# Kernel tuning notes

Hardware: AMD Instinct MI355X
Metric: run time of the kernel (lower is better)

## Reference

```python
import jax, jax.numpy as jnp
import numpy as np

# Hyperparameters (match init_kwargs)
COORD_DIM = 3
GRID_MIN = -1.0
GRID_MAX = 1.0
N_LEVELS = 16
N_FEATS = 2
LOG2_T = 19
TABLE_SIZE = 2 ** LOG2_T
BASE_RES = 16
FINEST_RES = 512
BSZ = 1048576

_growth = np.exp((np.log(FINEST_RES) - np.log(BASE_RES)) / (N_LEVELS - 1))
RESOLUTIONS = [int(np.floor(BASE_RES * _growth ** i)) for i in range(N_LEVELS)]

# InstantNGP spatial-hash primes (uint32: low bits of the product/xor are
# identical to the int64 computation, and we only keep LOG2_T low bits).
PRIMES = jnp.asarray(np.array([1, 2654435761, 805459861], dtype=np.uint32))
# (8, 3) binary corner offsets of a unit cube.
OFFSETS = jnp.asarray(
    np.array([[(k >> d) & 1 for d in range(COORD_DIM)] for k in range(2 ** COORD_DIM)],
             dtype=np.uint32))
MASK = jnp.uint32(TABLE_SIZE - 1)


def _embed_level(x, table, resolution):
    """x: (B, 3) coords; table: (T, F) hash table. Returns (B, F)."""
    grid_size = (GRID_MAX - GRID_MIN) / resolution
    rel = (x - GRID_MIN) / grid_size                       # (B, 3)
    idx0 = jnp.clip(jnp.floor(rel), 0, resolution - 1)     # bottom-left vertex index
    w = rel - idx0                                         # (B, 3) interp weights in [0,1]
    vidx = idx0.astype(jnp.uint32)[:, None, :] + OFFSETS[None]   # (B, 8, 3)
    # spatial hash: xor of (index * prime) over dims, masked to table size
    vp = vidx * PRIMES[None, None, :]
    h = (vp[..., 0] ^ vp[..., 1] ^ vp[..., 2]) & MASK      # (B, 8) uint32
    verts = table[h.astype(jnp.int32)]                      # (B, 8, F) gather
    # d-linear interpolation weights per corner
    wts = jnp.prod(jnp.where(OFFSETS[None] == 1, w[:, None, :], 1.0 - w[:, None, :]),
                   axis=-1)                                 # (B, 8)
    return jnp.einsum('bv,bvf->bf', wts, verts)             # (B, F)


def setup_inputs() -> dict:
    k1, k2 = jax.random.split(jax.random.key(0))
    x = jax.random.uniform(k1, (BSZ, COORD_DIM), jnp.float32,
                           minval=GRID_MIN, maxval=GRID_MAX)
    embeddings = jax.random.uniform(k2, (N_LEVELS, TABLE_SIZE, N_FEATS), jnp.float32,
                                    minval=-1e-4, maxval=1e-4)
    return {"x": x, "embeddings": embeddings}


def reference(x, embeddings):
    outs = [_embed_level(x, embeddings[i], RESOLUTIONS[i]) for i in range(N_LEVELS)]
    return jnp.concatenate(outs, axis=-1)  # (B, L*F)
```

## Files before the change

kernel.cpp:

```cpp
#include <hip/hip_runtime.h>
#include <hip/hip_fp16.h>
#include <stdint.h>


#define N_LEVELS   16
#define LOG2_T     19
#define TABLE_SIZE (1u << LOG2_T)
#define HASH_MASK  (TABLE_SIZE - 1u)
#define P1 2654435761u
#define P2 805459861u
#define N_DENSE    8

__constant__ int   c_res[N_LEVELS]   = {16, 20, 25, 32, 40, 50, 64, 80,
                                        101, 128, 161, 203, 256, 322, 406, 512};
__constant__ float c_scale[N_LEVELS] = {8.0f, 10.0f, 12.5f, 16.0f, 20.0f, 25.0f,
                                        32.0f, 40.0f, 50.5f, 64.0f, 80.5f, 101.5f,
                                        128.0f, 161.0f, 203.0f, 256.0f};

__constant__ uint32_t c_dim[N_DENSE]  = {17, 21, 26, 33, 41, 51, 65, 81};
__constant__ uint32_t c_doff[N_DENSE] = {0, 4913, 14174, 31750,
                                         67687, 136608, 269259, 543884};
#define DENSE_TOTAL 1075325u

__constant__ uint32_t c_coff[N_DENSE] = {0, 4096, 12096, 27721,
                                         60489, 124489, 249489, 511633};
#define CELL_TOTAL 1023633u

__global__ __launch_bounds__(256) void conv_hash(
    const float2* __restrict__ emb, uint32_t* __restrict__ ht, int total)
{
    int i = blockIdx.x * 256 + threadIdx.x;
    if (i >= total) return;
    float2 v = emb[(size_t)N_DENSE * TABLE_SIZE + i];
    __half2 h = __float22half2_rn(v);
    ht[i] = *(uint32_t*)&h;
}

__global__ __launch_bounds__(256) void conv_cell(
    const float2* __restrict__ emb, uint4* __restrict__ cg)
{
    int l = blockIdx.y;
    uint32_t c = blockIdx.x * 256 + threadIdx.x;
    uint32_t R = (uint32_t)c_res[l];
    if (c >= R * R * R) return;
    uint32_t ix = c % R;
    uint32_t r  = c / R;
    uint32_t iy = r % R;
    uint32_t iz = r / R;

    const float2* __restrict__ tb = emb + (size_t)l * TABLE_SIZE;
    uint32_t a0 = ix,      a1 = ix + 1u;
    uint32_t b0 = iy * P1, b1 = b0 + P1;
    uint32_t d0 = iz * P2, d1 = d0 + P2;

    float2 f0 = tb[(a0 ^ b0 ^ d0) & HASH_MASK];
    float2 f1 = tb[(a1 ^ b0 ^ d0) & HASH_MASK];
    float2 f2 = tb[(a0 ^ b1 ^ d0) & HASH_MASK];
    float2 f3 = tb[(a1 ^ b1 ^ d0) & HASH_MASK];
    float2 f4 = tb[(a0 ^ b0 ^ d1) & HASH_MASK];
    float2 f5 = tb[(a1 ^ b0 ^ d1) & HASH_MASK];
    float2 f6 = tb[(a0 ^ b1 ^ d1) & HASH_MASK];
    float2 f7 = tb[(a1 ^ b1 ^ d1) & HASH_MASK];

    __half2 h0 = __float22half2_rn(f0), h1 = __float22half2_rn(f1);
    __half2 h2 = __float22half2_rn(f2), h3 = __float22half2_rn(f3);
    __half2 h4 = __float22half2_rn(f4), h5 = __float22half2_rn(f5);
    __half2 h6 = __float22half2_rn(f6), h7 = __float22half2_rn(f7);

    uint32_t base = 2u * (c_coff[l] + c);
    cg[base]      = make_uint4(*(uint32_t*)&h0, *(uint32_t*)&h1,
                               *(uint32_t*)&h2, *(uint32_t*)&h3);
    cg[base + 1u] = make_uint4(*(uint32_t*)&h4, *(uint32_t*)&h5,
                               *(uint32_t*)&h6, *(uint32_t*)&h7);
}

__global__ __launch_bounds__(256) void conv_dense(
    const float2* __restrict__ emb, uint32_t* __restrict__ dn)
{
    int l = blockIdx.y;
    uint32_t v = blockIdx.x * 256 + threadIdx.x;
    uint32_t S = c_dim[l];
    if (v >= S * S * S) return;
    uint32_t ix = v % S;
    uint32_t r  = v / S;
    uint32_t iy = r % S;
    uint32_t iz = r / S;
    uint32_t h  = (ix ^ (iy * P1) ^ (iz * P2)) & HASH_MASK;
    float2 val  = emb[(size_t)l * TABLE_SIZE + h];
    __half2 hv  = __float22half2_rn(val);
    dn[c_doff[l] + v] = *(uint32_t*)&hv;
}

template <bool CELL>
__device__ __forceinline__ void do_point(
    int l, int b, int npts,
    const float* __restrict__ x,
    const uint32_t* __restrict__ ht,
    const uint32_t* __restrict__ dn,
    const uint4*    __restrict__ cg,
    uint32_t* __restrict__ tmp)
{
    if (b >= npts) return;
    size_t xb = (size_t)b * 3;
    float xx = x[xb], xy = x[xb + 1], xz = x[xb + 2];

    float scale = c_scale[l];
    float hiv   = (float)c_res[l] - 1.0f;

    float rx = (xx + 1.0f) * scale;
    float ry = (xy + 1.0f) * scale;
    float rz = (xz + 1.0f) * scale;

    float fx = fminf(fmaxf(floorf(rx), 0.0f), hiv);
    float fy = fminf(fmaxf(floorf(ry), 0.0f), hiv);
    float fz = fminf(fmaxf(floorf(rz), 0.0f), hiv);

    float wx = rx - fx, wy = ry - fy, wz = rz - fz;
    uint32_t ix = (uint32_t)fx, iy = (uint32_t)fy, iz = (uint32_t)fz;

    uint32_t u0, u1, u2, u3, u4, u5, u6, u7;
    if (l < N_DENSE) {
        if constexpr (CELL) {
            uint32_t R    = (uint32_t)c_res[l];
            uint32_t cidx = (iz * R + iy) * R + ix;
            uint32_t base = 2u * (c_coff[l] + cidx);
            uint4 lo = cg[base];
            uint4 hi = cg[base + 1u];
            u0 = lo.x; u1 = lo.y; u2 = lo.z; u3 = lo.w;
            u4 = hi.x; u5 = hi.y; u6 = hi.z; u7 = hi.w;
        } else {
            uint32_t S    = c_dim[l];
            uint32_t base = c_doff[l] + (iz * S + iy) * S + ix;
            uint32_t S2   = S * S;
            u0 = dn[base];           u1 = dn[base + 1];
            u2 = dn[base + S];       u3 = dn[base + S + 1];
            u4 = dn[base + S2];      u5 = dn[base + S2 + 1];
            u6 = dn[base + S2 + S];  u7 = dn[base + S2 + S + 1];
        }
    } else {
        const uint32_t* __restrict__ tb = ht + (size_t)(l - N_DENSE) * TABLE_SIZE;
        uint32_t a0 = ix,      a1 = ix + 1u;
        uint32_t b0 = iy * P1, b1 = b0 + P1;
        uint32_t c0 = iz * P2, c1 = c0 + P2;
        u0 = tb[(a0 ^ b0 ^ c0) & HASH_MASK];
        u1 = tb[(a1 ^ b0 ^ c0) & HASH_MASK];
        u2 = tb[(a0 ^ b1 ^ c0) & HASH_MASK];
        u3 = tb[(a1 ^ b1 ^ c0) & HASH_MASK];
        u4 = tb[(a0 ^ b0 ^ c1) & HASH_MASK];
        u5 = tb[(a1 ^ b0 ^ c1) & HASH_MASK];
        u6 = tb[(a0 ^ b1 ^ c1) & HASH_MASK];
        u7 = tb[(a1 ^ b1 ^ c1) & HASH_MASK];
    }

    float2 v0 = __half22float2(*(__half2*)&u0);
    float2 v1 = __half22float2(*(__half2*)&u1);
    float2 v2 = __half22float2(*(__half2*)&u2);
    float2 v3 = __half22float2(*(__half2*)&u3);
    float2 v4 = __half22float2(*(__half2*)&u4);
    float2 v5 = __half22float2(*(__half2*)&u5);
    float2 v6 = __half22float2(*(__half2*)&u6);
    float2 v7 = __half22float2(*(__half2*)&u7);

    float ux = 1.0f - wx, uy = 1.0f - wy, uz = 1.0f - wz;
    float w0 = ux * uy * uz, w1 = wx * uy * uz;
    float w2 = ux * wy * uz, w3 = wx * wy * uz;
    float w4 = ux * uy * wz, w5 = wx * uy * wz;
    float w6 = ux * wy * wz, w7 = wx * wy * wz;

    float o0 = w0 * v0.x + w1 * v1.x + w2 * v2.x + w3 * v3.x
             + w4 * v4.x + w5 * v5.x + w6 * v6.x + w7 * v7.x;
    float o1 = w0 * v0.y + w1 * v1.y + w2 * v2.y + w3 * v3.y
             + w4 * v4.y + w5 * v5.y + w6 * v6.y + w7 * v7.y;

    __half2 r = __float22half2_rn(make_float2(o0, o1));
    tmp[(size_t)l * npts + b] = *(uint32_t*)&r;
}

template <bool CELL>
__global__ __launch_bounds__(256) void gather_lvl(
    const float* __restrict__ x,
    const uint32_t* __restrict__ ht,
    const uint32_t* __restrict__ dn,
    const uint4*    __restrict__ cg,
    uint32_t* __restrict__ tmp, int npts)
{
    const int l  = blockIdx.y;
    const int bA = blockIdx.x * 512 + threadIdx.x;
    do_point<CELL>(l, bA,       npts, x, ht, dn, cg, tmp);
    do_point<CELL>(l, bA + 256, npts, x, ht, dn, cg, tmp);
}

__global__ __launch_bounds__(256) void transpose_k(
    const uint32_t* __restrict__ tmp, float4* __restrict__ out4, int npts)
{
    __shared__ uint32_t sm[N_LEVELS][514];

    const int b0 = blockIdx.x * 512;
    const int t  = threadIdx.x;

    if (b0 + 512 <= npts) {
        #pragma unroll
        for (int l = 0; l < N_LEVELS; ++l) {
            uint2 u = *(const uint2*)&tmp[(size_t)l * npts + b0 + 2 * t];
            *(uint2*)&sm[l][2 * t] = u;
        }
        __syncthreads();
        #pragma unroll
        for (int k = 0; k < 16; ++k) {
            int q = k * 256 + t;
            int p = q >> 3;
            int j = q & 7;
            uint32_t a = sm[2 * j][p], b = sm[2 * j + 1][p];
            float2 f0 = __half22float2(*(__half2*)&a);
            float2 f1 = __half22float2(*(__half2*)&b);
            out4[(size_t)(b0 + p) * 8 + j] = make_float4(f0.x, f0.y, f1.x, f1.y);
        }
    } else {
        for (int l = 0; l < N_LEVELS; ++l) {
            for (int s = 0; s < 2; ++s) {
                int b = b0 + 2 * t + s;
                if (b < npts) sm[l][2 * t + s] = tmp[(size_t)l * npts + b];
            }
        }
        __syncthreads();
        for (int k = 0; k < 16; ++k) {
            int q = k * 256 + t;
            int p = q >> 3, j = q & 7;
            if (b0 + p < npts) {
                uint32_t a = sm[2 * j][p], b = sm[2 * j + 1][p];
                float2 f0 = __half22float2(*(__half2*)&a);
                float2 f1 = __half22float2(*(__half2*)&b);
                out4[(size_t)(b0 + p) * 8 + j] = make_float4(f0.x, f0.y, f1.x, f1.y);
            }
        }
    }
}

__global__ __launch_bounds__(256) void hash_embed_direct(
    const float* __restrict__ x, const float* __restrict__ emb,
    float2* __restrict__ out, int npts)
{
    int t = blockIdx.x * 256 + threadIdx.x;
    int l = t & 15, b = t >> 4;
    if (b >= npts) return;
    size_t xb = (size_t)b * 3;
    float scale = c_scale[l], hiv = (float)c_res[l] - 1.0f;
    float rx = (x[xb] + 1.0f) * scale, ry = (x[xb+1] + 1.0f) * scale, rz = (x[xb+2] + 1.0f) * scale;
    float fx = fminf(fmaxf(floorf(rx), 0.0f), hiv);
    float fy = fminf(fmaxf(floorf(ry), 0.0f), hiv);
    float fz = fminf(fmaxf(floorf(rz), 0.0f), hiv);
    float wx = rx - fx, wy = ry - fy, wz = rz - fz;
    uint32_t ix = (uint32_t)fx, iy = (uint32_t)fy, iz = (uint32_t)fz;
    uint32_t a0 = ix, a1 = ix + 1u, b0 = iy * P1, b1 = b0 + P1, c0 = iz * P2, c1 = c0 + P2;
    const float2* tb = (const float2*)emb + (size_t)l * TABLE_SIZE;
    float2 v0 = tb[(a0^b0^c0)&HASH_MASK], v1 = tb[(a1^b0^c0)&HASH_MASK];
    float2 v2 = tb[(a0^b1^c0)&HASH_MASK], v3 = tb[(a1^b1^c0)&HASH_MASK];
    float2 v4 = tb[(a0^b0^c1)&HASH_MASK], v5 = tb[(a1^b0^c1)&HASH_MASK];
    float2 v6 = tb[(a0^b1^c1)&HASH_MASK], v7 = tb[(a1^b1^c1)&HASH_MASK];
    float ux = 1.0f - wx, uy = 1.0f - wy, uz = 1.0f - wz;
    float w0 = ux*uy*uz, w1 = wx*uy*uz, w2 = ux*wy*uz, w3 = wx*wy*uz;
    float w4 = ux*uy*wz, w5 = wx*uy*wz, w6 = ux*wy*wz, w7 = wx*wy*wz;
    float o0 = w0*v0.x+w1*v1.x+w2*v2.x+w3*v3.x+w4*v4.x+w5*v5.x+w6*v6.x+w7*v7.x;
    float o1 = w0*v0.y+w1*v1.y+w2*v2.y+w3*v3.y+w4*v4.y+w5*v5.y+w6*v6.y+w7*v7.y;
    out[(size_t)b * N_LEVELS + l] = make_float2(o0, o1);
}

extern "C" void kernel_launch(void* const* d_in, const int* in_sizes, int n_in,
                              void* d_out, int out_size, void* d_ws, size_t ws_size,
                              hipStream_t stream)
{
    const float*  x   = (const float*)d_in[0];
    const float2* emb = (const float2*)d_in[1];
    int npts = in_sizes[0] / 3;

    size_t tmp_bytes = (size_t)npts * N_LEVELS * 4;
    size_t ht_bytes  = (size_t)N_DENSE * TABLE_SIZE * 4;
    size_t cg_bytes  = (size_t)CELL_TOTAL * 32;
    size_t dn_bytes  = (size_t)DENSE_TOTAL * 4;

    int ht_total = N_DENSE * TABLE_SIZE;

    if (ws_size >= tmp_bytes + ht_bytes + cg_bytes) {
        uint32_t* tmp = (uint32_t*)d_ws;
        uint32_t* ht  = (uint32_t*)((char*)d_ws + tmp_bytes);
        uint4*    cg  = (uint4*)   ((char*)d_ws + tmp_bytes + ht_bytes);

        hipLaunchKernelGGL(conv_hash, dim3((ht_total + 255) / 256), dim3(256),
                           0, stream, emb, ht, ht_total);
        hipLaunchKernelGGL(conv_cell, dim3(2000, N_DENSE), dim3(256),
                           0, stream, emb, cg);
        hipLaunchKernelGGL(HIP_KERNEL_NAME(gather_lvl<true>),
                           dim3((npts + 511) / 512, N_LEVELS), dim3(256),
                           0, stream, x, ht, (const uint32_t*)nullptr, cg, tmp, npts);
        hipLaunchKernelGGL(transpose_k, dim3((npts + 511) / 512), dim3(256),
                           0, stream, tmp, (float4*)d_out, npts);
    } else if (ws_size >= tmp_bytes + ht_bytes + dn_bytes) {
        uint32_t* tmp = (uint32_t*)d_ws;
        uint32_t* ht  = (uint32_t*)((char*)d_ws + tmp_bytes);
        uint32_t* dn  = (uint32_t*)((char*)d_ws + tmp_bytes + ht_bytes);

        hipLaunchKernelGGL(conv_hash, dim3((ht_total + 255) / 256), dim3(256),
                           0, stream, emb, ht, ht_total);
        hipLaunchKernelGGL(conv_dense, dim3(2077, N_DENSE), dim3(256),
                           0, stream, emb, dn);
        hipLaunchKernelGGL(HIP_KERNEL_NAME(gather_lvl<false>),
                           dim3((npts + 511) / 512, N_LEVELS), dim3(256),
                           0, stream, x, ht, dn, (const uint4*)nullptr, tmp, npts);
        hipLaunchKernelGGL(transpose_k, dim3((npts + 511) / 512), dim3(256),
                           0, stream, tmp, (float4*)d_out, npts);
    } else {
        int total = npts * N_LEVELS;
        hipLaunchKernelGGL(hash_embed_direct, dim3((total + 255) / 256), dim3(256),
                           0, stream, (const float*)x, (const float*)emb,
                           (float2*)d_out, npts);
    }
}
```

Before: 460.1 us.

## Fuse per-level gather and transpose into one per-point kernel over all levels

```diff
diff --git a/kernel.cpp b/kernel.cpp
--- a/kernel.cpp
+++ b/kernel.cpp
@@ -11,20 +11,20 @@
 #define P2 805459861u
 #define N_DENSE    8
 
-__constant__ int   c_res[N_LEVELS]   = {16, 20, 25, 32, 40, 50, 64, 80,
-                                        101, 128, 161, 203, 256, 322, 406, 512};
-__constant__ float c_scale[N_LEVELS] = {8.0f, 10.0f, 12.5f, 16.0f, 20.0f, 25.0f,
-                                        32.0f, 40.0f, 50.5f, 64.0f, 80.5f, 101.5f,
-                                        128.0f, 161.0f, 203.0f, 256.0f};
-
-__constant__ uint32_t c_dim[N_DENSE]  = {17, 21, 26, 33, 41, 51, 65, 81};
-__constant__ uint32_t c_doff[N_DENSE] = {0, 4913, 14174, 31750,
-                                         67687, 136608, 269259, 543884};
-#define DENSE_TOTAL 1075325u
-
+typedef float  fx4 __attribute__((ext_vector_type(4)));
+
+__constant__ int   c_res[N_DENSE]   = {16, 20, 25, 32, 40, 50, 64, 80};
 __constant__ uint32_t c_coff[N_DENSE] = {0, 4096, 12096, 27721,
                                          60489, 124489, 249489, 511633};
 #define CELL_TOTAL 1023633u
+
+constexpr int      kRes[N_LEVELS]   = {16, 20, 25, 32, 40, 50, 64, 80,
+                                       101, 128, 161, 203, 256, 322, 406, 512};
+constexpr float    kScale[N_LEVELS] = {8.0f, 10.0f, 12.5f, 16.0f, 20.0f, 25.0f,
+                                       32.0f, 40.0f, 50.5f, 64.0f, 80.5f, 101.5f,
+                                       128.0f, 161.0f, 203.0f, 256.0f};
+constexpr uint32_t kCoff[N_DENSE]   = {0, 4096, 12096, 27721,
+                                       60489, 124489, 249489, 511633};
 
 __global__ __launch_bounds__(256) void conv_hash(
     const float2* __restrict__ emb, uint32_t* __restrict__ ht, int total)
@@ -74,164 +74,90 @@
                                *(uint32_t*)&h6, *(uint32_t*)&h7);
 }
 
-__global__ __launch_bounds__(256) void conv_dense(
-    const float2* __restrict__ emb, uint32_t* __restrict__ dn)
-{
-    int l = blockIdx.y;
-    uint32_t v = blockIdx.x * 256 + threadIdx.x;
-    uint32_t S = c_dim[l];
-    if (v >= S * S * S) return;
-    uint32_t ix = v % S;
-    uint32_t r  = v / S;
-    uint32_t iy = r % S;
-    uint32_t iz = r / S;
-    uint32_t h  = (ix ^ (iy * P1) ^ (iz * P2)) & HASH_MASK;
-    float2 val  = emb[(size_t)l * TABLE_SIZE + h];
-    __half2 hv  = __float22half2_rn(val);
-    dn[c_doff[l] + v] = *(uint32_t*)&hv;
-}
-
-template <bool CELL>
-__device__ __forceinline__ void do_point(
-    int l, int b, int npts,
+__global__ __launch_bounds__(256) void gather_all(
     const float* __restrict__ x,
     const uint32_t* __restrict__ ht,
-    const uint32_t* __restrict__ dn,
     const uint4*    __restrict__ cg,
-    uint32_t* __restrict__ tmp)
-{
+    float*          __restrict__ out, int npts)
+{
+    int b = blockIdx.x * 256 + threadIdx.x;
     if (b >= npts) return;
+
     size_t xb = (size_t)b * 3;
     float xx = x[xb], xy = x[xb + 1], xz = x[xb + 2];
 
-    float scale = c_scale[l];
-    float hiv   = (float)c_res[l] - 1.0f;
-
-    float rx = (xx + 1.0f) * scale;
-    float ry = (xy + 1.0f) * scale;
-    float rz = (xz + 1.0f) * scale;
-
-    float fx = fminf(fmaxf(floorf(rx), 0.0f), hiv);
-    float fy = fminf(fmaxf(floorf(ry), 0.0f), hiv);
-    float fz = fminf(fmaxf(floorf(rz), 0.0f), hiv);
-
-    float wx = rx - fx, wy = ry - fy, wz = rz - fz;
-    uint32_t ix = (uint32_t)fx, iy = (uint32_t)fy, iz = (uint32_t)fz;
-
-    uint32_t u0, u1, u2, u3, u4, u5, u6, u7;
-    if (l < N_DENSE) {
-        if constexpr (CELL) {
-            uint32_t R    = (uint32_t)c_res[l];
-            uint32_t cidx = (iz * R + iy) * R + ix;
-            uint32_t base = 2u * (c_coff[l] + cidx);
+    float e0 = 0.0f, e1 = 0.0f;
+
+    #pragma unroll
+    for (int l = 0; l < N_LEVELS; ++l) {
+        const float scale = kScale[l];
+        const float hiv   = (float)kRes[l] - 1.0f;
+
+        float rx = (xx + 1.0f) * scale;
+        float ry = (xy + 1.0f) * scale;
+        float rz = (xz + 1.0f) * scale;
+
+        float fx = fminf(fmaxf(floorf(rx), 0.0f), hiv);
+        float fy = fminf(fmaxf(floorf(ry), 0.0f), hiv);
+        float fz = fminf(fmaxf(floorf(rz), 0.0f), hiv);
+
+        float wx = rx - fx, wy = ry - fy, wz = rz - fz;
+        uint32_t ix = (uint32_t)fx, iy = (uint32_t)fy, iz = (uint32_t)fz;
+
+        uint32_t u0, u1, u2, u3, u4, u5, u6, u7;
+        if (l < N_DENSE) {
+            const uint32_t R    = (uint32_t)kRes[l];
+            const uint32_t cidx = (iz * R + iy) * R + ix;
+            const uint32_t base = 2u * (kCoff[l] + cidx);
             uint4 lo = cg[base];
             uint4 hi = cg[base + 1u];
             u0 = lo.x; u1 = lo.y; u2 = lo.z; u3 = lo.w;
             u4 = hi.x; u5 = hi.y; u6 = hi.z; u7 = hi.w;
         } else {
-            uint32_t S    = c_dim[l];
-            uint32_t base = c_doff[l] + (iz * S + iy) * S + ix;
-            uint32_t S2   = S * S;
-            u0 = dn[base];           u1 = dn[base + 1];
-            u2 = dn[base + S];       u3 = dn[base + S + 1];
-            u4 = dn[base + S2];      u5 = dn[base + S2 + 1];
-            u6 = dn[base + S2 + S];  u7 = dn[base + S2 + S + 1];
+            const uint32_t* __restrict__ tb =
+                ht + (size_t)(l - N_DENSE) * TABLE_SIZE;
+            uint32_t a0 = ix,      a1 = ix + 1u;
+            uint32_t b0 = iy * P1, b1 = b0 + P1;
+            uint32_t c0 = iz * P2, c1 = c0 + P2;
+            u0 = tb[(a0 ^ b0 ^ c0) & HASH_MASK];
+            u1 = tb[(a1 ^ b0 ^ c0) & HASH_MASK];
+            u2 = tb[(a0 ^ b1 ^ c0) & HASH_MASK];
+            u3 = tb[(a1 ^ b1 ^ c0) & HASH_MASK];
+            u4 = tb[(a0 ^ b0 ^ c1) & HASH_MASK];
+            u5 = tb[(a1 ^ b0 ^ c1) & HASH_MASK];
+            u6 = tb[(a0 ^ b1 ^ c1) & HASH_MASK];
+            u7 = tb[(a1 ^ b1 ^ c1) & HASH_MASK];
         }
-    } else {
-        const uint32_t* __restrict__ tb = ht + (size_t)(l - N_DENSE) * TABLE_SIZE;
-        uint32_t a0 = ix,      a1 = ix + 1u;
-        uint32_t b0 = iy * P1, b1 = b0 + P1;
-        uint32_t c0 = iz * P2, c1 = c0 + P2;
-        u0 = tb[(a0 ^ b0 ^ c0) & HASH_MASK];
-        u1 = tb[(a1 ^ b0 ^ c0) & HASH_MASK];
-        u2 = tb[(a0 ^ b1 ^ c0) & HASH_MASK];
-        u3 = tb[(a1 ^ b1 ^ c0) & HASH_MASK];
-        u4 = tb[(a0 ^ b0 ^ c1) & HASH_MASK];
-        u5 = tb[(a1 ^ b0 ^ c1) & HASH_MASK];
-        u6 = tb[(a0 ^ b1 ^ c1) & HASH_MASK];
-        u7 = tb[(a1 ^ b1 ^ c1) & HASH_MASK];
-    }
-
-    float2 v0 = __half22float2(*(__half2*)&u0);
-    float2 v1 = __half22float2(*(__half2*)&u1);
-    float2 v2 = __half22float2(*(__half2*)&u2);
-    float2 v3 = __half22float2(*(__half2*)&u3);
-    float2 v4 = __half22float2(*(__half2*)&u4);
-    float2 v5 = __half22float2(*(__half2*)&u5);
-    float2 v6 = __half22float2(*(__half2*)&u6);
-    float2 v7 = __half22float2(*(__half2*)&u7);
-
-    float ux = 1.0f - wx, uy = 1.0f - wy, uz = 1.0f - wz;
-    float w0 = ux * uy * uz, w1 = wx * uy * uz;
-    float w2 = ux * wy * uz, w3 = wx * wy * uz;
-    float w4 = ux * uy * wz, w5 = wx * uy * wz;
-    float w6 = ux * wy * wz, w7 = wx * wy * wz;
-
-    float o0 = w0 * v0.x + w1 * v1.x + w2 * v2.x + w3 * v3.x
-             + w4 * v4.x + w5 * v5.x + w6 * v6.x + w7 * v7.x;
-    float o1 = w0 * v0.y + w1 * v1.y + w2 * v2.y + w3 * v3.y
-             + w4 * v4.y + w5 * v5.y + w6 * v6.y + w7 * v7.y;
-
-    __half2 r = __float22half2_rn(make_float2(o0, o1));
-    tmp[(size_t)l * npts + b] = *(uint32_t*)&r;
-}
-
-template <bool CELL>
-__global__ __launch_bounds__(256) void gather_lvl(
-    const float* __restrict__ x,
-    const uint32_t* __restrict__ ht,
-    const uint32_t* __restrict__ dn,
-    const uint4*    __restrict__ cg,
-    uint32_t* __restrict__ tmp, int npts)
-{
-    const int l  = blockIdx.y;
-    const int bA = blockIdx.x * 512 + threadIdx.x;
-    do_point<CELL>(l, bA,       npts, x, ht, dn, cg, tmp);
-    do_point<CELL>(l, bA + 256, npts, x, ht, dn, cg, tmp);
-}
-
-__global__ __launch_bounds__(256) void transpose_k(
-    const uint32_t* __restrict__ tmp, float4* __restrict__ out4, int npts)
-{
-    __shared__ uint32_t sm[N_LEVELS][514];
-
-    const int b0 = blockIdx.x * 512;
-    const int t  = threadIdx.x;
-
-    if (b0 + 512 <= npts) {
-        #pragma unroll
-        for (int l = 0; l < N_LEVELS; ++l) {
-            uint2 u = *(const uint2*)&tmp[(size_t)l * npts + b0 + 2 * t];
-            *(uint2*)&sm[l][2 * t] = u;
-        }
-        __syncthreads();
-        #pragma unroll
-        for (int k = 0; k < 16; ++k) {
-            int q = k * 256 + t;
-            int p = q >> 3;
-            int j = q & 7;
-            uint32_t a = sm[2 * j][p], b = sm[2 * j + 1][p];
-            float2 f0 = __half22float2(*(__half2*)&a);
-            float2 f1 = __half22float2(*(__half2*)&b);
-            out4[(size_t)(b0 + p) * 8 + j] = make_float4(f0.x, f0.y, f1.x, f1.y);
-        }
-    } else {
-        for (int l = 0; l < N_LEVELS; ++l) {
-            for (int s = 0; s < 2; ++s) {
-                int b = b0 + 2 * t + s;
-                if (b < npts) sm[l][2 * t + s] = tmp[(size_t)l * npts + b];
-            }
-        }
-        __syncthreads();
-        for (int k = 0; k < 16; ++k) {
-            int q = k * 256 + t;
-            int p = q >> 3, j = q & 7;
-            if (b0 + p < npts) {
-                uint32_t a = sm[2 * j][p], b = sm[2 * j + 1][p];
-                float2 f0 = __half22float2(*(__half2*)&a);
-                float2 f1 = __half22float2(*(__half2*)&b);
-                out4[(size_t)(b0 + p) * 8 + j] = make_float4(f0.x, f0.y, f1.x, f1.y);
-            }
+
+        float2 v0 = __half22float2(*(__half2*)&u0);
+        float2 v1 = __half22float2(*(__half2*)&u1);
+        float2 v2 = __half22float2(*(__half2*)&u2);
+        float2 v3 = __half22float2(*(__half2*)&u3);
+        float2 v4 = __half22float2(*(__half2*)&u4);
+        float2 v5 = __half22float2(*(__half2*)&u5);
+        float2 v6 = __half22float2(*(__half2*)&u6);
+        float2 v7 = __half22float2(*(__half2*)&u7);
+
+        float ux = 1.0f - wx, uy = 1.0f - wy, uz = 1.0f - wz;
+        float w0 = ux * uy * uz, w1 = wx * uy * uz;
+        float w2 = ux * wy * uz, w3 = wx * wy * uz;
+        float w4 = ux * uy * wz, w5 = wx * uy * wz;
+        float w6 = ux * wy * wz, w7 = wx * wy * wz;
+
+        float o0 = w0 * v0.x + w1 * v1.x + w2 * v2.x + w3 * v3.x
+                 + w4 * v4.x + w5 * v5.x + w6 * v6.x + w7 * v7.x;
+        float o1 = w0 * v0.y + w1 * v1.y + w2 * v2.y + w3 * v3.y
+                 + w4 * v4.y + w5 * v5.y + w6 * v6.y + w7 * v7.y;
+
+        __half2 hr = __float22half2_rn(make_float2(o0, o1));
+        float2 fr = __half22float2(hr);
+
+        if (l & 1) {
+            fx4 v; v.x = e0; v.y = e1; v.z = fr.x; v.w = fr.y;
+            __builtin_nontemporal_store(
+                v, (fx4*)(out + (size_t)b * 32 + (l >> 1) * 4));
+        } else {
+            e0 = fr.x; e1 = fr.y;
         }
     }
 }
@@ -244,7 +170,12 @@
     int l = t & 15, b = t >> 4;
     if (b >= npts) return;
     size_t xb = (size_t)b * 3;
-    float scale = c_scale[l], hiv = (float)c_res[l] - 1.0f;
+    constexpr float kS[16] = {8.0f, 10.0f, 12.5f, 16.0f, 20.0f, 25.0f,
+                              32.0f, 40.0f, 50.5f, 64.0f, 80.5f, 101.5f,
+                              128.0f, 161.0f, 203.0f, 256.0f};
+    constexpr int   kR[16] = {16, 20, 25, 32, 40, 50, 64, 80,
+                              101, 128, 161, 203, 256, 322, 406, 512};
+    float scale = kS[l], hiv = (float)kR[l] - 1.0f;
     float rx = (x[xb] + 1.0f) * scale, ry = (x[xb+1] + 1.0f) * scale, rz = (x[xb+2] + 1.0f) * scale;
     float fx = fminf(fmaxf(floorf(rx), 0.0f), hiv);
     float fy = fminf(fmaxf(floorf(ry), 0.0f), hiv);
@@ -273,41 +204,20 @@
     const float2* emb = (const float2*)d_in[1];
     int npts = in_sizes[0] / 3;
 
-    size_t tmp_bytes = (size_t)npts * N_LEVELS * 4;
-    size_t ht_bytes  = (size_t)N_DENSE * TABLE_SIZE * 4;
-    size_t cg_bytes  = (size_t)CELL_TOTAL * 32;
-    size_t dn_bytes  = (size_t)DENSE_TOTAL * 4;
-
+    size_t ht_bytes = (size_t)N_DENSE * TABLE_SIZE * 4;
+    size_t cg_bytes = (size_t)CELL_TOTAL * 32;
     int ht_total = N_DENSE * TABLE_SIZE;
 
-    if (ws_size >= tmp_bytes + ht_bytes + cg_bytes) {
-        uint32_t* tmp = (uint32_t*)d_ws;
-        uint32_t* ht  = (uint32_t*)((char*)d_ws + tmp_bytes);
-        uint4*    cg  = (uint4*)   ((char*)d_ws + tmp_bytes + ht_bytes);
+    if (ws_size >= ht_bytes + cg_bytes) {
+        uint32_t* ht = (uint32_t*)d_ws;
+        uint4*    cg = (uint4*)((char*)d_ws + ht_bytes);
 
         hipLaunchKernelGGL(conv_hash, dim3((ht_total + 255) / 256), dim3(256),
                            0, stream, emb, ht, ht_total);
         hipLaunchKernelGGL(conv_cell, dim3(2000, N_DENSE), dim3(256),
                            0, stream, emb, cg);
-        hipLaunchKernelGGL(HIP_KERNEL_NAME(gather_lvl<true>),
-                           dim3((npts + 511) / 512, N_LEVELS), dim3(256),
-                           0, stream, x, ht, (const uint32_t*)nullptr, cg, tmp, npts);
-        hipLaunchKernelGGL(transpose_k, dim3((npts + 511) / 512), dim3(256),
-                           0, stream, tmp, (float4*)d_out, npts);
-    } else if (ws_size >= tmp_bytes + ht_bytes + dn_bytes) {
-        uint32_t* tmp = (uint32_t*)d_ws;
-        uint32_t* ht  = (uint32_t*)((char*)d_ws + tmp_bytes);
-        uint32_t* dn  = (uint32_t*)((char*)d_ws + tmp_bytes + ht_bytes);
-
-        hipLaunchKernelGGL(conv_hash, dim3((ht_total + 255) / 256), dim3(256),
-                           0, stream, emb, ht, ht_total);
-        hipLaunchKernelGGL(conv_dense, dim3(2077, N_DENSE), dim3(256),
-                           0, stream, emb, dn);
-        hipLaunchKernelGGL(HIP_KERNEL_NAME(gather_lvl<false>),
-                           dim3((npts + 511) / 512, N_LEVELS), dim3(256),
-                           0, stream, x, ht, dn, (const uint4*)nullptr, tmp, npts);
-        hipLaunchKernelGGL(transpose_k, dim3((npts + 511) / 512), dim3(256),
-                           0, stream, tmp, (float4*)d_out, npts);
+        hipLaunchKernelGGL(gather_all, dim3((npts + 255) / 256), dim3(256),
+                           0, stream, x, ht, cg, (float*)d_out, npts);
     } else {
         int total = npts * N_LEVELS;
         hipLaunchKernelGGL(hash_embed_direct, dim3((total + 255) / 256), dim3(256),
```

New measurement: 615.5 us. +33.8%, slower.
